# Performance work log

Hardware: AMD Instinct MI355X
Metric: run time of the kernel (lower is better)

## Reference

```python
import jax, jax.numpy as jnp
import numpy as np

N = 30000
E = 480000
D_IN = 128
EPS = 1e-5
NEG_SLOPE = 0.2
# (in_dim, out_channels, heads) per GATConv layer; concat=True everywhere (PyG default)
CFG = [(D_IN, 100, 5), (500, 50, 5), (250, 32, 4), (128, 8, 4), (32, 1, 1)]
BN_DIMS = (500, 250, 128)


def setup_inputs() -> dict:
    key = jax.random.key(0)
    ks = iter(jax.random.split(key, 80))
    inp = {
        "x": jax.random.normal(next(ks), (N, D_IN), jnp.float32),
        "edge_index": jax.random.randint(next(ks), (2, E), 0, N),
        "edge_weight": jax.random.uniform(next(ks), (E, 1), jnp.float32),
    }
    for l, (cin, cout, h) in enumerate(CFG, 1):
        s = 1.0 / np.sqrt(cin)
        inp[f"W{l}"] = jax.random.normal(next(ks), (cin, h * cout), jnp.float32) * s
        inp[f"a_s{l}"] = jax.random.normal(next(ks), (1, h, cout), jnp.float32) * 0.1
        inp[f"a_d{l}"] = jax.random.normal(next(ks), (1, h, cout), jnp.float32) * 0.1
        inp[f"We{l}"] = jax.random.normal(next(ks), (1, h * cout), jnp.float32)
        inp[f"a_e{l}"] = jax.random.normal(next(ks), (1, h, cout), jnp.float32) * 0.1
        inp[f"b{l}"] = jnp.zeros((h * cout,), jnp.float32)
    for l, d in zip((1, 2, 3), BN_DIMS):
        inp[f"g{l}"] = jnp.ones((d,), jnp.float32)
        inp[f"beta{l}"] = jnp.zeros((d,), jnp.float32)
    return inp


def _gat(x, src, dst, ea, W, a_s, a_d, We, a_e, b, heads, cout):
    """PyG GATConv with edge_dim attention (concat=True)."""
    n = x.shape[0]
    h = (x @ W).reshape(n, heads, cout)            # [N,H,C]
    e = (ea @ We).reshape(-1, heads, cout)         # [E,H,C]
    al_src = (h * a_s).sum(-1)                     # [N,H]
    al_dst = (h * a_d).sum(-1)                     # [N,H]
    logit = jax.nn.leaky_relu(al_src[src] + al_dst[dst] + (e * a_e).sum(-1), NEG_SLOPE)
    m = jax.ops.segment_max(logit, dst, num_segments=n)
    m = jnp.where(jnp.isfinite(m), m, 0.0)
    ex = jnp.exp(logit - m[dst])                   # [E,H]
    den = jax.ops.segment_sum(ex, dst, num_segments=n)
    alpha = ex / jnp.maximum(den[dst], 1e-16)      # segment softmax over in-edges of dst
    out = jax.ops.segment_sum(h[src] * alpha[..., None], dst, num_segments=n)
    return out.reshape(n, heads * cout) + b


def _bn(x, g, b):
    mu = x.mean(0)
    var = x.var(0)  # biased, as torch uses for normalization
    return (x - mu) * jax.lax.rsqrt(var + EPS) * g + b


def reference(x, edge_index, edge_weight,
              W1, a_s1, a_d1, We1, a_e1, b1,
              W2, a_s2, a_d2, We2, a_e2, b2,
              W3, a_s3, a_d3, We3, a_e3, b3,
              W4, a_s4, a_d4, We4, a_e4, b4,
              W5, a_s5, a_d5, We5, a_e5, b5,
              g1, beta1, g2, beta2, g3, beta3):
    # add self loops (PyG default) with edge_attr fill_value='mean'
    loop = jnp.arange(N)
    src = jnp.concatenate([edge_index[0], loop])
    dst = jnp.concatenate([edge_index[1], loop])
    ea = jnp.concatenate([edge_weight, jnp.full((N, 1), edge_weight.mean(), edge_weight.dtype)], axis=0)

    h = _gat(x, src, dst, ea, W1, a_s1, a_d1, We1, a_e1, b1, 5, 100)
    h = jax.nn.relu(_bn(h, g1, beta1))
    h = _gat(h, src, dst, ea, W2, a_s2, a_d2, We2, a_e2, b2, 5, 50)
    h = jax.nn.relu(_bn(h, g2, beta2))
    h = _gat(h, src, dst, ea, W3, a_s3, a_d3, We3, a_e3, b3, 4, 32)
    h = jax.nn.relu(_bn(h, g3, beta3))
    h = _gat(h, src, dst, ea, W4, a_s4, a_d4, We4, a_e4, b4, 4, 8)
    h = jax.nn.relu(h)
    h = _gat(h, src, dst, ea, W5, a_s5, a_d5, We5, a_e5, b5, 1, 1)
    return h
```

## Files before the change

### kernel.cpp

```cpp
#include <hip/hip_runtime.h>
#include <hip/hip_bf16.h>
#include <math.h>

#define NN 30000
#define EE 480000
#define ET (EE + NN)
#define NEG_SLOPE 0.2f
#define BN_EPS 1e-5f

struct LayerCfg { int cin, C, H; };
static const LayerCfg g_cfg[5] = {
    {128, 100, 5}, {500, 50, 5}, {250, 32, 4}, {128, 8, 4}, {32, 1, 1}
};

typedef short short8 __attribute__((ext_vector_type(8)));
typedef float f32x4 __attribute__((ext_vector_type(4)));

__device__ __forceinline__ unsigned short f2bf(float f) {
    unsigned int u = __builtin_bit_cast(unsigned int, f);
    u = (u + 0x7FFFu + ((u >> 16) & 1u)) >> 16;
    return (unsigned short)u;
}
__device__ __forceinline__ float bf2f(unsigned short h) {
    unsigned int u = ((unsigned int)h) << 16;
    return __builtin_bit_cast(float, u);
}


struct PrepArgs {
    const float* W[5];
    const float* We[5];
    const float* ae[5];
    unsigned short* bh[5];
    unsigned short* bl[5];
    float* wedot;
    int K[5], N[5], Kp[5], Np[5], C[5], H[5];
};

static const int EBLK = (ET + 255) / 256;

__global__ void prep_fused_kernel(const int* __restrict__ ei, int* __restrict__ rank,
                                  int* __restrict__ cnt, const float* __restrict__ ew,
                                  float* __restrict__ esum, PrepArgs a) {
    __shared__ float sdata[256];
    __shared__ float tile[32][33];
    int b = blockIdx.x;
    int tid = threadIdx.x;

    if (b < EBLK) {
        int e = b * 256 + tid;
        if (e < ET) {
            int d = (e < EE) ? ei[EE + e] : (e - EE);
            rank[e] = atomicAdd(&cnt[d], 1);
        }
        return;
    }
    b -= EBLK;
    if (b < 256) {
        float s = 0.f;
        for (int i = b * 256 + tid; i < EE; i += 65536)
            s += ew[i];
        sdata[tid] = s;
        __syncthreads();
        for (int off = 128; off > 0; off >>= 1) {
            if (tid < off) sdata[tid] += sdata[tid + off];
            __syncthreads();
        }
        if (tid == 0) atomicAdd(esum, sdata[0]);
        return;
    }
    b -= 256;
    int bx = b & 15, by = (b >> 4) & 15, bz = b >> 8;
    int l = bz;
    int tx = tid & 31, ty = tid >> 5;
    if (bx == 0 && by == 0 && ty == 0 && tx < 8) {
        int hd = tx;
        if (hd < a.H[l]) {
            int C = a.C[l];
            const float* We = a.We[l] + hd * C;
            const float* ae = a.ae[l] + hd * C;
            float s = 0.f;
            for (int c = 0; c < C; c++) s += We[c] * ae[c];
            a.wedot[l * 8 + hd] = s;
        }
    }
    int Kp = a.Kp[l], Np = a.Np[l], K = a.K[l], N = a.N[l];
    int kb = bx * 32, nb = by * 32;
    if (kb >= Kp || nb >= Np) return;
    const float* B = a.W[l];
    unsigned short* Bth = a.bh[l];
    unsigned short* Btl = a.bl[l];
#pragma unroll
    for (int i = 0; i < 4; i++) {
        int k = kb + ty + i * 8, n = nb + tx;
        tile[ty + i * 8][tx] = (k < K && n < N) ? B[(size_t)k * N + n] : 0.f;
    }
    __syncthreads();
#pragma unroll
    for (int i = 0; i < 4; i++) {
        int n = nb + ty + i * 8, k = kb + tx;
        if (n < Np && k < Kp) {
            float v = tile[tx][ty + i * 8];
            unsigned short hi = f2bf(v);
            unsigned short lo = f2bf(v - bf2f(hi));
            size_t idx = (size_t)n * Kp + k;
            Bth[idx] = hi;
            Btl[idx] = lo;
        }
    }
}

__global__ void scan_kernel(const int* __restrict__ cnt, int* __restrict__ off) {
    __shared__ int lsum[1024];
    const int T = 1024;
    int t = threadIdx.x;
    int chunk = (NN + T - 1) / T;
    int base = t * chunk;
    int end = min(NN, base + chunk);
    int s = 0;
    for (int i = base; i < end; i++) s += cnt[i];
    lsum[t] = s;
    __syncthreads();
    for (int d = 1; d < T; d <<= 1) {
        int v = (t >= d) ? lsum[t - d] : 0;
        __syncthreads();
        lsum[t] += v;
        __syncthreads();
    }
    int run = (t == 0) ? 0 : lsum[t - 1];
    for (int i = base; i < end; i++) {
        off[i] = run;
        run += cnt[i];
    }
    if (t == 0) off[NN] = ET;
}

__global__ void fill_kernel(const int* __restrict__ ei, const int* __restrict__ rank,
                            const float* __restrict__ ew, const float* __restrict__ esum,
                            const int* __restrict__ off,
                            int* __restrict__ csr_src, float* __restrict__ csr_ea) {
    int e = blockIdx.x * blockDim.x + threadIdx.x;
    if (e >= ET) return;
    int sv, d;
    if (e < EE) { sv = ei[e]; d = ei[EE + e]; }
    else        { sv = e - EE; d = e - EE; }
    int p = off[d] + rank[e];
    csr_src[p] = sv;
    csr_ea[p]  = (e < EE) ? ew[e] : esum[0] * (1.0f / (float)EE);
}

#define GBM 128
#define GBNT 128
#define GBK 32
#define ASTR 36
__global__ __launch_bounds__(256) void gemm_split_kernel(const float* __restrict__ A,
                                                         const unsigned short* __restrict__ Bt_hi,
                                                         const unsigned short* __restrict__ Bt_lo,
                                                         float* __restrict__ Cm,
                                                         unsigned short* __restrict__ Ch16,
                                                         int M, int Kp, int Nc,
                                                         const float* __restrict__ colsum,
                                                         const float* __restrict__ colsumsq,
                                                         const float* __restrict__ g,
                                                         const float* __restrict__ beta,
                                                         int D) {
    __shared__ short AsH[GBM * ASTR];
    __shared__ short AsL[GBM * ASTR];
    __shared__ short BsH[GBNT * ASTR];
    __shared__ short BsL[GBNT * ASTR];
    __shared__ float sscale[512];
    __shared__ float sshift[512];
    int tid = threadIdx.x;
    bool bn = (colsum != nullptr);
    if (bn) {
        for (int c = tid; c < Kp; c += 256) {
            float sc = 0.f, sh = 0.f;
            if (c < D) {
                float mu = colsum[c] * (1.0f / (float)NN);
                float var = colsumsq[c] * (1.0f / (float)NN) - mu * mu;
                sc = g[c] * rsqrtf(var + BN_EPS);
                sh = beta[c] - mu * sc;
            }
            sscale[c] = sc;
            sshift[c] = sh;
        }
        __syncthreads();
    }
    int wave = tid >> 6, lane = tid & 63;
    int q = lane >> 4, r = lane & 15;
    int m0 = blockIdx.y * GBM, n0 = blockIdx.x * GBNT;
    int wm = (wave & 1) * 64, wn = (wave >> 1) * 64;
    f32x4 acc[4][4];
#pragma unroll
    for (int i = 0; i < 4; i++)
#pragma unroll
        for (int j = 0; j < 4; j++) acc[i][j] = (f32x4)(0.f);

    int arow2 = tid >> 1;
    int acol2 = (tid & 1) * 16;
    int brow = tid >> 2;
    int bcol = (tid & 3) * 8;

    int ksteps = Kp / GBK;
    for (int ks = 0; ks < ksteps; ks++) {
        int k0 = ks * GBK;
        {
            int m = m0 + arow2;
            float v[16];
            if (m < M) {
                const float* Ap = A + (size_t)m * Kp + k0 + acol2;
                float4 f0 = *(const float4*)(Ap);
                float4 f1 = *(const float4*)(Ap + 4);
                float4 f2 = *(const float4*)(Ap + 8);
                float4 f3 = *(const float4*)(Ap + 12);
                v[0]=f0.x; v[1]=f0.y; v[2]=f0.z; v[3]=f0.w;
                v[4]=f1.x; v[5]=f1.y; v[6]=f1.z; v[7]=f1.w;
                v[8]=f2.x; v[9]=f2.y; v[10]=f2.z; v[11]=f2.w;
                v[12]=f3.x; v[13]=f3.y; v[14]=f3.z; v[15]=f3.w;
                if (bn) {
                    int cb = k0 + acol2;
#pragma unroll
                    for (int i = 0; i < 16; i++)
                        v[i] = fmaxf(v[i] * sscale[cb + i] + sshift[cb + i], 0.f);
                }
            } else {
#pragma unroll
                for (int i = 0; i < 16; i++) v[i] = 0.f;
            }
#pragma unroll
            for (int i = 0; i < 16; i++) {
                unsigned short hi = f2bf(v[i]);
                unsigned short lo = f2bf(v[i] - bf2f(hi));
                AsH[arow2 * ASTR + acol2 + i] = (short)hi;
                AsL[arow2 * ASTR + acol2 + i] = (short)lo;
            }
        }
#pragma unroll
        for (int p = 0; p < 2; p++) {
            int row = p * 64 + brow;
            size_t gidx = (size_t)(n0 + row) * Kp + k0 + bcol;
            *((uint4*)(BsH + row * ASTR + bcol)) = *((const uint4*)(Bt_hi + gidx));
            *((uint4*)(BsL + row * ASTR + bcol)) = *((const uint4*)(Bt_lo + gidx));
        }
        __syncthreads();
        short8 ah[4], al[4], bh[4], bl[4];
#pragma unroll
        for (int i = 0; i < 4; i++) {
            ah[i] = *((const short8*)(AsH + (wm + i * 16 + r) * ASTR + q * 8));
            al[i] = *((const short8*)(AsL + (wm + i * 16 + r) * ASTR + q * 8));
        }
#pragma unroll
        for (int j = 0; j < 4; j++) {
            bh[j] = *((const short8*)(BsH + (wn + j * 16 + r) * ASTR + q * 8));
            bl[j] = *((const short8*)(BsL + (wn + j * 16 + r) * ASTR + q * 8));
        }
#pragma unroll
        for (int i = 0; i < 4; i++)
#pragma unroll
            for (int j = 0; j < 4; j++) {
                acc[i][j] = __builtin_amdgcn_mfma_f32_16x16x32_bf16(ah[i], bh[j], acc[i][j], 0, 0, 0);
                acc[i][j] = __builtin_amdgcn_mfma_f32_16x16x32_bf16(ah[i], bl[j], acc[i][j], 0, 0, 0);
                acc[i][j] = __builtin_amdgcn_mfma_f32_16x16x32_bf16(al[i], bh[j], acc[i][j], 0, 0, 0);
            }
        __syncthreads();
    }
#pragma unroll
    for (int i = 0; i < 4; i++) {
#pragma unroll
        for (int j = 0; j < 4; j++) {
#pragma unroll
            for (int reg = 0; reg < 4; reg++) {
                int mrow = m0 + wm + i * 16 + q * 4 + reg;
                int ncol = n0 + wn + j * 16 + r;
                if (mrow < M && ncol < Nc) {
                    float val = acc[i][j][reg];
                    if (Cm)   Cm[(size_t)mrow * Nc + ncol] = val;
                    if (Ch16) Ch16[(size_t)mrow * Nc + ncol] = f2bf(val);
                }
            }
        }
    }
}

__global__ void gemv_l5_kernel(const float* __restrict__ X, const float* __restrict__ W,
                               const float* __restrict__ a_s, const float* __restrict__ a_d,
                               float* __restrict__ h, float* __restrict__ al_src,
                               float* __restrict__ al_dst) {
    __shared__ float w[32];
    if (threadIdx.x < 32) w[threadIdx.x] = W[threadIdx.x];
    __syncthreads();
    int n = blockIdx.x * blockDim.x + threadIdx.x;
    if (n >= NN) return;
    const float* row = X + (size_t)n * 32;
    float s = 0.f;
#pragma unroll
    for (int i = 0; i < 8; i++) {
        float4 f = *(const float4*)(row + i * 4);
        s += f.x * w[i * 4] + f.y * w[i * 4 + 1] + f.z * w[i * 4 + 2] + f.w * w[i * 4 + 3];
    }
    h[n] = s;
    al_src[n] = s * a_s[0];
    al_dst[n] = s * a_d[0];
}

__global__ void al_wave_h16_kernel(const unsigned short* __restrict__ h16,
                                   const float* __restrict__ a_s,
                                   const float* __restrict__ a_d,
                                   float* __restrict__ al_src, float* __restrict__ al_dst,
                                   int H, int C, int HCp) {
    int w = (blockIdx.x * blockDim.x + threadIdx.x) >> 6;
    int lane = threadIdx.x & 63;
    if (w >= NN) return;
    const unsigned short* row = h16 + (size_t)w * HCp;
    float s1[5] = {0.f, 0.f, 0.f, 0.f, 0.f};
    float s2[5] = {0.f, 0.f, 0.f, 0.f, 0.f};
#pragma unroll
    for (int hd = 0; hd < 5; hd++) {
        if (hd >= H) break;
        int base = hd * C;
        for (int c = lane * 2; c < C; c += 128) {
            unsigned int u = *(const unsigned int*)(row + base + c);
            float v0 = bf2f((unsigned short)(u & 0xffffu));
            float v1 = bf2f((unsigned short)(u >> 16));
            s1[hd] += v0 * a_s[base + c] + v1 * a_s[base + c + 1];
            s2[hd] += v0 * a_d[base + c] + v1 * a_d[base + c + 1];
        }
    }
#pragma unroll
    for (int hd = 0; hd < 5; hd++) {
        if (hd >= H) break;
#pragma unroll
        for (int off = 32; off > 0; off >>= 1) {
            s1[hd] += __shfl_xor(s1[hd], off, 64);
            s2[hd] += __shfl_xor(s2[hd], off, 64);
        }
    }
    if (lane == 0) {
#pragma unroll
        for (int hd = 0; hd < 5; hd++) {
            if (hd >= H) break;
            al_src[(size_t)w * H + hd] = s1[hd];
            al_dst[(size_t)w * H + hd] = s2[hd];
        }
    }
}

__global__ void attn_kernel(const float* __restrict__ al_src,
                            const float* __restrict__ al_dst,
                            const int* __restrict__ csr_src,
                            const float* __restrict__ csr_ea,
                            const float* __restrict__ we_dot,
                            const int* __restrict__ off,
                            float* __restrict__ alpha_t,
                            float* __restrict__ inv_den, int H, int NH) {
    int t = blockIdx.x * blockDim.x + threadIdx.x;
    if (t >= NH) return;
    int n = t / H, hd = t - n * H;
    int s = off[n], e = off[n + 1];
    float ad = al_dst[(size_t)n * H + hd];
    float wd = we_dot[hd];
    float* arow = alpha_t + (size_t)hd * ET;
    float den = 0.f;
    int p = s;
    for (; p + 3 < e; p += 4) {
        int s0 = csr_src[p], s1 = csr_src[p + 1], s2 = csr_src[p + 2], s3 = csr_src[p + 3];
        float w0 = csr_ea[p], w1 = csr_ea[p + 1], w2 = csr_ea[p + 2], w3 = csr_ea[p + 3];
        float l0 = al_src[(size_t)s0 * H + hd] + ad + w0 * wd;
        float l1 = al_src[(size_t)s1 * H + hd] + ad + w1 * wd;
        float l2 = al_src[(size_t)s2 * H + hd] + ad + w2 * wd;
        float l3 = al_src[(size_t)s3 * H + hd] + ad + w3 * wd;
        l0 = (l0 >= 0.f) ? l0 : NEG_SLOPE * l0;
        l1 = (l1 >= 0.f) ? l1 : NEG_SLOPE * l1;
        l2 = (l2 >= 0.f) ? l2 : NEG_SLOPE * l2;
        l3 = (l3 >= 0.f) ? l3 : NEG_SLOPE * l3;
        float e0 = __expf(l0), e1 = __expf(l1), e2 = __expf(l2), e3 = __expf(l3);
        arow[p] = e0; arow[p + 1] = e1; arow[p + 2] = e2; arow[p + 3] = e3;
        den += e0 + e1 + e2 + e3;
    }
    for (; p < e; p++) {
        float lg = al_src[(size_t)csr_src[p] * H + hd] + ad + csr_ea[p] * wd;
        lg = (lg >= 0.f) ? lg : NEG_SLOPE * lg;
        float ex = __expf(lg);
        arow[p] = ex;
        den += ex;
    }
    inv_den[t] = 1.f / fmaxf(den, 1e-16f);
}

#define AGG_T 64
#define IDX_STR 68
#define AL_ROW 68
__global__ void aggregate_slab_lds_kernel(const unsigned short* __restrict__ h16,
                                          const float* __restrict__ alpha_t,
                                          const int* __restrict__ off,
                                          const int* __restrict__ csr_src,
                                          const float* __restrict__ bias,
                                          const float* __restrict__ inv_den,
                                          float* __restrict__ out,
                                          int C, int H, int HC, int hp,
                                          int lns, int lcps, int npr, int nhs,
                                          int algstr, int tight, int relu, int opitch) {
    extern __shared__ char smem[];
    int cps = 1 << lcps;
    int G = 256 >> lcps;
    int* sidx = (int*)smem;
    float* sal = (float*)(smem + (size_t)G * IDX_STR * 4);
    __shared__ int s_maxt;

    int vs = blockIdx.x & 7;
    int nb = blockIdx.x >> 3;
    int slab = vs & ((1 << lns) - 1);
    int rep  = vs >> lns;
    int tid = threadIdx.x;
    int lc = tid & (cps - 1);
    int g = tid >> lcps;
    int nl = nb * G + g;
    bool active = (nl < npr);
    int n = rep * npr + (active ? nl : 0);

    int slab_j = slab << (lcps + 2);
    int j = slab_j + (lc << 2);
    int hlo = slab_j / C;
    int hhi = (slab_j + (cps << 2) - 1) / C;
    if (hhi > H - 1) hhi = H - 1;
    int nval = hhi - hlo + 1;

    int hdA = j / C;
    int hdB = (j + 3) / C;
    int bnd = (hdA + 1) * C - j;
    bnd = (bnd > 4) ? 4 : bnd;
    int selA = hdA - hlo; if (selA >= nhs) selA = nhs - 1;
    int selB = hdB - hlo; if (selB >= nhs) selB = nhs - 1;
    int hA = (hdA < H) ? hdA : H - 1;
    int hB = (hdB < H) ? hdB : H - 1;

    int s = active ? off[n] : 0;
    int e = active ? off[n + 1] : 0;
    int nt = (e - s + AGG_T - 1) / AGG_T;

    if (tid == 0) s_maxt = 0;
    __syncthreads();
    if (lc == 0 && active && nt > 0) atomicMax(&s_maxt, nt);
    __syncthreads();
    int maxt = s_maxt;

    int hpb = hp << 1;
    const char* hb = (const char*)(h16 + j);
    int* myidx = sidx + g * IDX_STR;
    float* myal = sal + (size_t)g * algstr;
    float ac0 = 0.f, ac1 = 0.f, ac2 = 0.f, ac3 = 0.f;

    for (int t = 0; t < maxt; t++) {
        int base = s + t * AGG_T;
        int cnt = e - base;
        if (cnt < 0) cnt = 0;
        if (cnt > AGG_T) cnt = AGG_T;
        __syncthreads();
        for (int q = lc; q < cnt; q += cps)
            myidx[q] = csr_src[base + q] * hpb;
        for (int r = 0; r < nhs; r++) {
            bool hv = (r < nval);
            const float* ar = alpha_t + (size_t)(hlo + r) * ET;
            float* dst = myal + r * AL_ROW;
            for (int q = lc; q < cnt; q += cps)
                dst[q] = hv ? ar[base + q] : 0.f;
        }
        __syncthreads();
        if (tight) {
            const float* aA = myal + selA * AL_ROW;
            int q = 0;
            for (; q + 3 < cnt; q += 4) {
                int b0 = myidx[q], b1 = myidx[q + 1], b2 = myidx[q + 2], b3 = myidx[q + 3];
                float a0 = aA[q], a1 = aA[q + 1], a2 = aA[q + 2], a3 = aA[q + 3];
                ushort4 u0 = *(const ushort4*)(hb + b0);
                ushort4 u1 = *(const ushort4*)(hb + b1);
                ushort4 u2 = *(const ushort4*)(hb + b2);
                ushort4 u3 = *(const ushort4*)(hb + b3);
                ac0 += a0 * bf2f(u0.x); ac1 += a0 * bf2f(u0.y);
                ac2 += a0 * bf2f(u0.z); ac3 += a0 * bf2f(u0.w);
                ac0 += a1 * bf2f(u1.x); ac1 += a1 * bf2f(u1.y);
                ac2 += a1 * bf2f(u1.z); ac3 += a1 * bf2f(u1.w);
                ac0 += a2 * bf2f(u2.x); ac1 += a2 * bf2f(u2.y);
                ac2 += a2 * bf2f(u2.z); ac3 += a2 * bf2f(u2.w);
                ac0 += a3 * bf2f(u3.x); ac1 += a3 * bf2f(u3.y);
                ac2 += a3 * bf2f(u3.z); ac3 += a3 * bf2f(u3.w);
            }
            for (; q < cnt; q++) {
                int b0 = myidx[q];
                float a0 = aA[q];
                ushort4 uv = *(const ushort4*)(hb + b0);
                ac0 += a0 * bf2f(uv.x); ac1 += a0 * bf2f(uv.y);
                ac2 += a0 * bf2f(uv.z); ac3 += a0 * bf2f(uv.w);
            }
        } else {
            const float* aA = myal + selA * AL_ROW;
            const float* aB = myal + selB * AL_ROW;
            int q = 0;
            for (; q + 3 < cnt; q += 4) {
                int b0 = myidx[q], b1 = myidx[q + 1], b2 = myidx[q + 2], b3 = myidx[q + 3];
                float a0 = aA[q], a1 = aA[q + 1], a2 = aA[q + 2], a3 = aA[q + 3];
                float c0 = aB[q], c1 = aB[q + 1], c2 = aB[q + 2], c3 = aB[q + 3];
                ushort4 u0 = *(const ushort4*)(hb + b0);
                ushort4 u1 = *(const ushort4*)(hb + b1);
                ushort4 u2 = *(const ushort4*)(hb + b2);
                ushort4 u3 = *(const ushort4*)(hb + b3);
                ac0 += ((0 < bnd) ? a0 : c0) * bf2f(u0.x);
                ac1 += ((1 < bnd) ? a0 : c0) * bf2f(u0.y);
                ac2 += ((2 < bnd) ? a0 : c0) * bf2f(u0.z);
                ac3 += ((3 < bnd) ? a0 : c0) * bf2f(u0.w);
                ac0 += ((0 < bnd) ? a1 : c1) * bf2f(u1.x);
                ac1 += ((1 < bnd) ? a1 : c1) * bf2f(u1.y);
                ac2 += ((2 < bnd) ? a1 : c1) * bf2f(u1.z);
                ac3 += ((3 < bnd) ? a1 : c1) * bf2f(u1.w);
                ac0 += ((0 < bnd) ? a2 : c2) * bf2f(u2.x);
                ac1 += ((1 < bnd) ? a2 : c2) * bf2f(u2.y);
                ac2 += ((2 < bnd) ? a2 : c2) * bf2f(u2.z);
                ac3 += ((3 < bnd) ? a2 : c2) * bf2f(u2.w);
                ac0 += ((0 < bnd) ? a3 : c3) * bf2f(u3.x);
                ac1 += ((1 < bnd) ? a3 : c3) * bf2f(u3.y);
                ac2 += ((2 < bnd) ? a3 : c3) * bf2f(u3.z);
                ac3 += ((3 < bnd) ? a3 : c3) * bf2f(u3.w);
            }
            for (; q < cnt; q++) {
                int b0 = myidx[q];
                float a0 = aA[q], c0 = aB[q];
                ushort4 uv = *(const ushort4*)(hb + b0);
                ac0 += ((0 < bnd) ? a0 : c0) * bf2f(uv.x);
                ac1 += ((1 < bnd) ? a0 : c0) * bf2f(uv.y);
                ac2 += ((2 < bnd) ? a0 : c0) * bf2f(uv.z);
                ac3 += ((3 < bnd) ? a0 : c0) * bf2f(uv.w);
            }
        }
    }
    if (!active) return;
    float invA = inv_den[(size_t)n * H + hA];
    float invB = inv_den[(size_t)n * H + hB];
    float o0 = ac0 * ((0 < bnd) ? invA : invB) + ((j + 0 < HC) ? bias[j + 0] : 0.f);
    float o1 = ac1 * ((1 < bnd) ? invA : invB) + ((j + 1 < HC) ? bias[j + 1] : 0.f);
    float o2 = ac2 * ((2 < bnd) ? invA : invB) + ((j + 2 < HC) ? bias[j + 2] : 0.f);
    float o3 = ac3 * ((3 < bnd) ? invA : invB) + ((j + 3 < HC) ? bias[j + 3] : 0.f);
    if (relu) {
        o0 = fmaxf(o0, 0.f); o1 = fmaxf(o1, 0.f);
        o2 = fmaxf(o2, 0.f); o3 = fmaxf(o3, 0.f);
    }
    *(float4*)(out + (size_t)n * opitch + j) = make_float4(o0, o1, o2, o3);
}

__global__ void aggregate_kernel(const float* __restrict__ hfeat,
                                 const float* __restrict__ alpha_t,
                                 const int* __restrict__ off, const int* __restrict__ csr_src,
                                 const float* __restrict__ bias,
                                 const float* __restrict__ inv_den,
                                 float* __restrict__ out, int total) {
    int t = blockIdx.x * blockDim.x + threadIdx.x;
    if (t >= total) return;
    int n = t;
    int s = off[n], e = off[n + 1];
    float acc = 0.f;
    int p = s;
    for (; p + 3 < e; p += 4) {
        acc += alpha_t[p] * hfeat[csr_src[p]]
             + alpha_t[p + 1] * hfeat[csr_src[p + 1]]
             + alpha_t[p + 2] * hfeat[csr_src[p + 2]]
             + alpha_t[p + 3] * hfeat[csr_src[p + 3]];
    }
    for (; p < e; p++) acc += alpha_t[p] * hfeat[csr_src[p]];
    out[n] = acc * inv_den[n] + bias[0];
}


__global__ void bn_stats_kernel(const float* __restrict__ x, float* __restrict__ colsum,
                                float* __restrict__ colsumsq, int D, int pitch) {
    int rows_per_block = (NN + gridDim.x - 1) / gridDim.x;
    int r0 = blockIdx.x * rows_per_block;
    int r1 = min(NN, r0 + rows_per_block);
    int c0 = threadIdx.x;
    int c1 = threadIdx.x + 256;
    float s0 = 0.f, q0 = 0.f, s1 = 0.f, q1 = 0.f;
    for (int r = r0; r < r1; r++) {
        const float* row = x + (size_t)r * pitch;
        if (c0 < D) { float v = row[c0]; s0 += v; q0 += v * v; }
        if (c1 < D) { float v = row[c1]; s1 += v; q1 += v * v; }
    }
    if (c0 < D) { atomicAdd(&colsum[c0], s0); atomicAdd(&colsumsq[c0], q0); }
    if (c1 < D) { atomicAdd(&colsum[c1], s1); atomicAdd(&colsumsq[c1], q1); }
}


static inline size_t align_up(size_t v, size_t a) { return (v + a - 1) / a * a; }

extern "C" void kernel_launch(void* const* d_in, const int* in_sizes, int n_in,
                              void* d_out, int out_size, void* d_ws, size_t ws_size,
                              hipStream_t stream) {
    const float* x_in = (const float*)d_in[0];
    const int* ei     = (const int*)d_in[1];
    const float* ew   = (const float*)d_in[2];

    char* pws = (char*)d_ws;
    size_t off_b = 0;
    auto alloc = [&](size_t bytes) -> void* {
        void* rp = pws + off_b;
        off_b = align_up(off_b + bytes, 256);
        return rp;
    };
    float* B0      = (float*)alloc((size_t)NN * 4);
    float* B1      = (float*)alloc((size_t)NN * 512 * 4);
    unsigned short* H16 = (unsigned short*)alloc((size_t)NN * 512 * 2);
    float* alpha_t = (float*)alloc((size_t)ET * 5 * 4);
    unsigned short* Wt_hi = (unsigned short*)alloc((size_t)600 * 512 * 2);
    unsigned short* Wt_lo = (unsigned short*)alloc((size_t)600 * 512 * 2);
    float* al_src  = (float*)alloc((size_t)NN * 5 * 4);
    float* al_dst  = (float*)alloc((size_t)NN * 5 * 4);
    float* inv_den = (float*)alloc((size_t)NN * 5 * 4);
    float* csr_ea  = (float*)alloc((size_t)ET * 4);
    int* rankb     = (int*)alloc((size_t)ET * 4);
    int* csr_src   = (int*)alloc((size_t)ET * 4);
    int* offarr    = (int*)alloc((size_t)(NN + 1) * 4);
    float* we_dot  = (float*)alloc(40 * 4);
    float* esum    = (float*)alloc(4);
    int* cnt       = (int*)alloc((size_t)NN * 4);
    float* colsum_all   = (float*)alloc(3 * 512 * 4);
    float* colsumsq_all = (float*)alloc(3 * 512 * 4);
    char* zero_end = pws + off_b;
    (void)ws_size; (void)n_in; (void)in_sizes; (void)out_size;

    int Kp[5], Np[5], hp[5];
    size_t wtoff[5];
    size_t acc_off = 0;
    for (int l = 0; l < 5; l++) {
        int K = g_cfg[l].cin, HC = g_cfg[l].C * g_cfg[l].H;
        Kp[l] = (K + 31) / 32 * 32;
        Np[l] = (HC + 127) / 128 * 128;
        hp[l] = (HC >= 64) ? ((HC + 63) / 64 * 64) : ((HC + 7) / 8 * 8);
        wtoff[l] = acc_off;
        acc_off += (size_t)Kp[l] * Np[l];
    }

    PrepArgs pa;
    for (int l = 0; l < 5; l++) {
        pa.W[l]  = (const float*)d_in[3 + l * 6 + 0];
        pa.We[l] = (const float*)d_in[3 + l * 6 + 3];
        pa.ae[l] = (const float*)d_in[3 + l * 6 + 4];
        pa.bh[l] = Wt_hi + wtoff[l];
        pa.bl[l] = Wt_lo + wtoff[l];
        pa.K[l] = g_cfg[l].cin;
        pa.N[l] = g_cfg[l].C * g_cfg[l].H;
        pa.Kp[l] = Kp[l];
        pa.Np[l] = Np[l];
        pa.C[l] = g_cfg[l].C;
        pa.H[l] = g_cfg[l].H;
    }
    pa.wedot = we_dot;

    hipMemsetAsync(esum, 0, (size_t)(zero_end - (char*)esum), stream);
    int ebl = EBLK;
    prep_fused_kernel<<<ebl + 256 + 1280, 256, 0, stream>>>(ei, rankb, cnt, ew, esum, pa);
    scan_kernel<<<1, 1024, 0, stream>>>(cnt, offarr);
    fill_kernel<<<ebl, 256, 0, stream>>>(ei, rankb, ew, esum, offarr, csr_src, csr_ea);

    for (int l = 0; l < 5; l++) {
        const LayerCfg& cf = g_cfg[l];
        int H = cf.H, C = cf.C;
        int HC = H * C;
        const float* a_s = (const float*)d_in[3 + l * 6 + 1];
        const float* a_d = (const float*)d_in[3 + l * 6 + 2];
        const float* b   = (const float*)d_in[3 + l * 6 + 5];

        const float* X = (l == 0) ? x_in : B1;
        float* outbuf = (l == 4) ? (float*)d_out : B1;
        int opitch = (l == 4) ? 1 : Kp[l + 1];
        int NH = NN * H;
        int alblocks = (NN * 64 + 255) / 256;

        if (l == 4) {
            gemv_l5_kernel<<<(NN + 255) / 256, 256, 0, stream>>>(
                X, pa.W[4], a_s, a_d, B0, al_src, al_dst);
        } else {
            const float* cs = (l >= 1) ? colsum_all + (l - 1) * 512 : nullptr;
            const float* cq = (l >= 1) ? colsumsq_all + (l - 1) * 512 : nullptr;
            const float* gg = (l >= 1) ? (const float*)d_in[33 + (l - 1) * 2 + 0] : nullptr;
            const float* bb = (l >= 1) ? (const float*)d_in[33 + (l - 1) * 2 + 1] : nullptr;
            int Din = (l >= 1) ? g_cfg[l - 1].C * g_cfg[l - 1].H : 0;
            dim3 ggrid(Np[l] / GBNT, (NN + GBM - 1) / GBM);
            gemm_split_kernel<<<ggrid, 256, 0, stream>>>(X, Wt_hi + wtoff[l], Wt_lo + wtoff[l],
                                                         nullptr, H16,
                                                         NN, Kp[l], hp[l], cs, cq, gg, bb, Din);
            al_wave_h16_kernel<<<alblocks, 256, 0, stream>>>(H16, a_s, a_d, al_src, al_dst, H, C, hp[l]);
        }

        attn_kernel<<<(NH + 255) / 256, 256, 0, stream>>>(al_src, al_dst, csr_src, csr_ea,
                                                          we_dot + l * 8, offarr, alpha_t,
                                                          inv_den, H, NH);

        if (l == 4) {
            aggregate_kernel<<<(NN + 255) / 256, 256, 0, stream>>>(
                B0, alpha_t, offarr, csr_src, b, inv_den, outbuf, NN);
        } else {
            int cps = (hp[l] >= 64) ? 16 : 8;
            int lcps = (cps == 16) ? 4 : 3;
            int slabcols = cps * 4;
            int nslabs = hp[l] / slabcols;
            int lns = (nslabs == 8) ? 3 : (nslabs == 4) ? 2 : (nslabs == 2) ? 1 : 0;
            int dup = 8 / nslabs;
            int npr = NN / dup;
            int G = 256 / cps;
            int gx = 8 * ((npr + G - 1) / G);
            int nhs = 1;
            for (int sbi = 0; sbi < nslabs; sbi++) {
                int j0 = sbi * slabcols;
                int span = (j0 + slabcols - 1) / C - j0 / C + 1;
                if (span > nhs) nhs = span;
            }
            int algstr = nhs * AL_ROW + 4;
            int tight = ((C & 3) == 0) ? 1 : 0;
            size_t smem = (size_t)G * IDX_STR * 4 + (size_t)G * algstr * 4;
            aggregate_slab_lds_kernel<<<gx, 256, smem, stream>>>(
                H16, alpha_t, offarr, csr_src, b, inv_den, outbuf,
                C, H, HC, hp[l], lns, lcps, npr, nhs, algstr, tight,
                (l == 3) ? 1 : 0, opitch);
        }

        if (l < 3) {
            bn_stats_kernel<<<512, 256, 0, stream>>>(outbuf, colsum_all + l * 512,
                                                     colsumsq_all + l * 512, HC, opitch);
        }
    }
}
```

Measured before the change: 742.3 us.

## Fuse BN column statistics into aggregation and add 8-wide slab kernel for layer 3

Removes the separate bn_stats pass by accumulating per-column sum and sum-of-squares in LDS atomics inside the aggregation kernels, then flushing them to global with atomics. This saves a full re-read of each layer output. It also adds an aggregation variant for layer 3 where each lane gathers 8 bf16 columns with 16-byte loads. The cost is extra LDS atomic contention and a block-wide sync at the end of aggregation, plus global float atomics that make the summation order nondeterministic.

```diff
diff --git a/kernel.cpp b/kernel.cpp
--- a/kernel.cpp
+++ b/kernel.cpp
@@ -24,6 +24,12 @@
 __device__ __forceinline__ float bf2f(unsigned short h) {
     unsigned int u = ((unsigned int)h) << 16;
     return __builtin_bit_cast(float, u);
+}
+__device__ __forceinline__ float bf_lo(unsigned int d) {
+    return __builtin_bit_cast(float, d << 16);
+}
+__device__ __forceinline__ float bf_hi(unsigned int d) {
+    return __builtin_bit_cast(float, d & 0xffff0000u);
 }
 
 
@@ -399,13 +405,18 @@
                                           float* __restrict__ out,
                                           int C, int H, int HC, int hp,
                                           int lns, int lcps, int npr, int nhs,
-                                          int algstr, int tight, int relu, int opitch) {
+                                          int algstr, int tight,
+                                          float* __restrict__ cs_out,
+                                          float* __restrict__ cq_out,
+                                          int relu, int opitch) {
     extern __shared__ char smem[];
     int cps = 1 << lcps;
     int G = 256 >> lcps;
     int* sidx = (int*)smem;
     float* sal = (float*)(smem + (size_t)G * IDX_STR * 4);
     __shared__ int s_maxt;
+    __shared__ float bn_s[64];
+    __shared__ float bn_q[64];
 
     int vs = blockIdx.x & 7;
     int nb = blockIdx.x >> 3;
@@ -439,6 +450,7 @@
     int nt = (e - s + AGG_T - 1) / AGG_T;
 
     if (tid == 0) s_maxt = 0;
+    if (tid < 64) { bn_s[tid] = 0.f; bn_q[tid] = 0.f; }
     __syncthreads();
     if (lc == 0 && active && nt > 0) atomicMax(&s_maxt, nt);
     __syncthreads();
@@ -532,18 +544,171 @@
             }
         }
     }
-    if (!active) return;
     float invA = inv_den[(size_t)n * H + hA];
     float invB = inv_den[(size_t)n * H + hB];
     float o0 = ac0 * ((0 < bnd) ? invA : invB) + ((j + 0 < HC) ? bias[j + 0] : 0.f);
     float o1 = ac1 * ((1 < bnd) ? invA : invB) + ((j + 1 < HC) ? bias[j + 1] : 0.f);
     float o2 = ac2 * ((2 < bnd) ? invA : invB) + ((j + 2 < HC) ? bias[j + 2] : 0.f);
     float o3 = ac3 * ((3 < bnd) ? invA : invB) + ((j + 3 < HC) ? bias[j + 3] : 0.f);
+    if (cs_out) {
+        if (active) {
+            int cb = lc << 2;
+            atomicAdd(&bn_s[cb + 0], o0); atomicAdd(&bn_q[cb + 0], o0 * o0);
+            atomicAdd(&bn_s[cb + 1], o1); atomicAdd(&bn_q[cb + 1], o1 * o1);
+            atomicAdd(&bn_s[cb + 2], o2); atomicAdd(&bn_q[cb + 2], o2 * o2);
+            atomicAdd(&bn_s[cb + 3], o3); atomicAdd(&bn_q[cb + 3], o3 * o3);
+        }
+        __syncthreads();
+        int sc = 1 << (lcps + 2);
+        if (tid < sc) {
+            atomicAdd(&cs_out[slab_j + tid], bn_s[tid]);
+            atomicAdd(&cq_out[slab_j + tid], bn_q[tid]);
+        }
+    }
+    if (!active) return;
     if (relu) {
         o0 = fmaxf(o0, 0.f); o1 = fmaxf(o1, 0.f);
         o2 = fmaxf(o2, 0.f); o3 = fmaxf(o3, 0.f);
     }
     *(float4*)(out + (size_t)n * opitch + j) = make_float4(o0, o1, o2, o3);
+}
+
+__global__ void aggregate_slab8_kernel(const unsigned short* __restrict__ h16,
+                                       const float* __restrict__ alpha_t,
+                                       const int* __restrict__ off,
+                                       const int* __restrict__ csr_src,
+                                       const float* __restrict__ bias,
+                                       const float* __restrict__ inv_den,
+                                       float* __restrict__ out,
+                                       int C, int H, int HC, int hp,
+                                       int lns, int npr, int nhs, int algstr,
+                                       float* __restrict__ cs_out,
+                                       float* __restrict__ cq_out,
+                                       int relu, int opitch) {
+    extern __shared__ char smem[];
+    const int cps = 8, G = 32;
+    int* sidx = (int*)smem;
+    float* sal = (float*)(smem + (size_t)G * IDX_STR * 4);
+    __shared__ int s_maxt;
+    __shared__ float bn_s[64];
+    __shared__ float bn_q[64];
+
+    int vs = blockIdx.x & 7;
+    int nb = blockIdx.x >> 3;
+    int slab = vs & ((1 << lns) - 1);
+    int rep  = vs >> lns;
+    int tid = threadIdx.x;
+    int lc = tid & 7;
+    int g = tid >> 3;
+    int nl = nb * G + g;
+    bool active = (nl < npr);
+    int n = rep * npr + (active ? nl : 0);
+
+    int slab_j = slab << 6;
+    int j = slab_j + (lc << 3);
+    int hlo = slab_j / C;
+    int hd = j / C;
+    int sel = hd - hlo; if (sel >= nhs) sel = nhs - 1;
+    int hcl = (hd < H) ? hd : H - 1;
+
+    int s = active ? off[n] : 0;
+    int e = active ? off[n + 1] : 0;
+    int nt = (e - s + AGG_T - 1) / AGG_T;
+    int hhi = (slab_j + 63) / C;
+    if (hhi > H - 1) hhi = H - 1;
+    int nval = hhi - hlo + 1;
+
+    if (tid == 0) s_maxt = 0;
+    if (tid < 64) { bn_s[tid] = 0.f; bn_q[tid] = 0.f; }
+    __syncthreads();
+    if (lc == 0 && active && nt > 0) atomicMax(&s_maxt, nt);
+    __syncthreads();
+    int maxt = s_maxt;
+
+    int hpb = hp << 1;
+    const char* hb = (const char*)(h16 + j);
+    int* myidx = sidx + g * IDX_STR;
+    float* myal = sal + (size_t)g * algstr;
+    float ac0 = 0.f, ac1 = 0.f, ac2 = 0.f, ac3 = 0.f;
+    float ac4 = 0.f, ac5 = 0.f, ac6 = 0.f, ac7 = 0.f;
+
+    for (int t = 0; t < maxt; t++) {
+        int base = s + t * AGG_T;
+        int cnt = e - base;
+        if (cnt < 0) cnt = 0;
+        if (cnt > AGG_T) cnt = AGG_T;
+        __syncthreads();
+        for (int q = lc; q < cnt; q += cps)
+            myidx[q] = csr_src[base + q] * hpb;
+        for (int r = 0; r < nhs; r++) {
+            bool hv = (r < nval);
+            const float* ar = alpha_t + (size_t)(hlo + r) * ET;
+            float* dst = myal + r * AL_ROW;
+            for (int q = lc; q < cnt; q += cps)
+                dst[q] = hv ? ar[base + q] : 0.f;
+        }
+        __syncthreads();
+        const float* aA = myal + sel * AL_ROW;
+        int q = 0;
+        for (; q + 1 < cnt; q += 2) {
+            int b0 = myidx[q], b1 = myidx[q + 1];
+            float a0 = aA[q], a1 = aA[q + 1];
+            uint4 u0 = *(const uint4*)(hb + b0);
+            uint4 u1 = *(const uint4*)(hb + b1);
+            ac0 += a0 * bf_lo(u0.x); ac1 += a0 * bf_hi(u0.x);
+            ac2 += a0 * bf_lo(u0.y); ac3 += a0 * bf_hi(u0.y);
+            ac4 += a0 * bf_lo(u0.z); ac5 += a0 * bf_hi(u0.z);
+            ac6 += a0 * bf_lo(u0.w); ac7 += a0 * bf_hi(u0.w);
+            ac0 += a1 * bf_lo(u1.x); ac1 += a1 * bf_hi(u1.x);
+            ac2 += a1 * bf_lo(u1.y); ac3 += a1 * bf_hi(u1.y);
+            ac4 += a1 * bf_lo(u1.z); ac5 += a1 * bf_hi(u1.z);
+            ac6 += a1 * bf_lo(u1.w); ac7 += a1 * bf_hi(u1.w);
+        }
+        for (; q < cnt; q++) {
+            int b0 = myidx[q];
+            float a0 = aA[q];
+            uint4 uv = *(const uint4*)(hb + b0);
+            ac0 += a0 * bf_lo(uv.x); ac1 += a0 * bf_hi(uv.x);
+            ac2 += a0 * bf_lo(uv.y); ac3 += a0 * bf_hi(uv.y);
+            ac4 += a0 * bf_lo(uv.z); ac5 += a0 * bf_hi(uv.z);
+            ac6 += a0 * bf_lo(uv.w); ac7 += a0 * bf_hi(uv.w);
+        }
+    }
+    float inv = inv_den[(size_t)n * H + hcl];
+    float o0 = ac0 * inv + ((j + 0 < HC) ? bias[j + 0] : 0.f);
+    float o1 = ac1 * inv + ((j + 1 < HC) ? bias[j + 1] : 0.f);
+    float o2 = ac2 * inv + ((j + 2 < HC) ? bias[j + 2] : 0.f);
+    float o3 = ac3 * inv + ((j + 3 < HC) ? bias[j + 3] : 0.f);
+    float o4 = ac4 * inv + ((j + 4 < HC) ? bias[j + 4] : 0.f);
+    float o5 = ac5 * inv + ((j + 5 < HC) ? bias[j + 5] : 0.f);
+    float o6 = ac6 * inv + ((j + 6 < HC) ? bias[j + 6] : 0.f);
+    float o7 = ac7 * inv + ((j + 7 < HC) ? bias[j + 7] : 0.f);
+    if (cs_out) {
+        if (active) {
+            int cb = lc << 3;
+            atomicAdd(&bn_s[cb + 0], o0); atomicAdd(&bn_q[cb + 0], o0 * o0);
+            atomicAdd(&bn_s[cb + 1], o1); atomicAdd(&bn_q[cb + 1], o1 * o1);
+            atomicAdd(&bn_s[cb + 2], o2); atomicAdd(&bn_q[cb + 2], o2 * o2);
+            atomicAdd(&bn_s[cb + 3], o3); atomicAdd(&bn_q[cb + 3], o3 * o3);
+            atomicAdd(&bn_s[cb + 4], o4); atomicAdd(&bn_q[cb + 4], o4 * o4);
+            atomicAdd(&bn_s[cb + 5], o5); atomicAdd(&bn_q[cb + 5], o5 * o5);
+            atomicAdd(&bn_s[cb + 6], o6); atomicAdd(&bn_q[cb + 6], o6 * o6);
+            atomicAdd(&bn_s[cb + 7], o7); atomicAdd(&bn_q[cb + 7], o7 * o7);
+        }
+        __syncthreads();
+        if (tid < 64) {
+            atomicAdd(&cs_out[slab_j + tid], bn_s[tid]);
+            atomicAdd(&cq_out[slab_j + tid], bn_q[tid]);
+        }
+    }
+    if (!active) return;
+    if (relu) {
+        o0 = fmaxf(o0, 0.f); o1 = fmaxf(o1, 0.f); o2 = fmaxf(o2, 0.f); o3 = fmaxf(o3, 0.f);
+        o4 = fmaxf(o4, 0.f); o5 = fmaxf(o5, 0.f); o6 = fmaxf(o6, 0.f); o7 = fmaxf(o7, 0.f);
+    }
+    float* op = out + (size_t)n * opitch + j;
+    *(float4*)(op)     = make_float4(o0, o1, o2, o3);
+    *(float4*)(op + 4) = make_float4(o4, o5, o6, o7);
 }
 
 __global__ void aggregate_kernel(const float* __restrict__ hfeat,
@@ -566,24 +731,6 @@
     }
     for (; p < e; p++) acc += alpha_t[p] * hfeat[csr_src[p]];
     out[n] = acc * inv_den[n] + bias[0];
-}
-
-
-__global__ void bn_stats_kernel(const float* __restrict__ x, float* __restrict__ colsum,
-                                float* __restrict__ colsumsq, int D, int pitch) {
-    int rows_per_block = (NN + gridDim.x - 1) / gridDim.x;
-    int r0 = blockIdx.x * rows_per_block;
-    int r1 = min(NN, r0 + rows_per_block);
-    int c0 = threadIdx.x;
-    int c1 = threadIdx.x + 256;
-    float s0 = 0.f, q0 = 0.f, s1 = 0.f, q1 = 0.f;
-    for (int r = r0; r < r1; r++) {
-        const float* row = x + (size_t)r * pitch;
-        if (c0 < D) { float v = row[c0]; s0 += v; q0 += v * v; }
-        if (c1 < D) { float v = row[c1]; s1 += v; q1 += v * v; }
-    }
-    if (c0 < D) { atomicAdd(&colsum[c0], s0); atomicAdd(&colsumsq[c0], q0); }
-    if (c1 < D) { atomicAdd(&colsum[c1], s1); atomicAdd(&colsumsq[c1], q1); }
 }
 
 
@@ -692,9 +839,30 @@
                                                           we_dot + l * 8, offarr, alpha_t,
                                                           inv_den, H, NH);
 
+        float* csO = (l < 3) ? colsum_all + l * 512 : nullptr;
+        float* cqO = (l < 3) ? colsumsq_all + l * 512 : nullptr;
+
         if (l == 4) {
             aggregate_kernel<<<(NN + 255) / 256, 256, 0, stream>>>(
                 B0, alpha_t, offarr, csr_src, b, inv_den, outbuf, NN);
+        } else if (l == 2) {
+            int nslabs = hp[l] / 64;
+            int lns = (nslabs == 2) ? 1 : 0;
+            int dup = 8 / nslabs;
+            int npr = NN / dup;
+            int G = 32;
+            int gx = 8 * ((npr + G - 1) / G);
+            int nhs = 1;
+            for (int sbi = 0; sbi < nslabs; sbi++) {
+                int j0 = sbi * 64;
+                int span = (j0 + 63) / C - j0 / C + 1;
+                if (span > nhs) nhs = span;
+            }
+            int algstr = nhs * AL_ROW + 4;
+            size_t smem = (size_t)G * IDX_STR * 4 + (size_t)G * algstr * 4;
+            aggregate_slab8_kernel<<<gx, 256, smem, stream>>>(
+                H16, alpha_t, offarr, csr_src, b, inv_den, outbuf,
+                C, H, HC, hp[l], lns, npr, nhs, algstr, csO, cqO, 0, opitch);
         } else {
             int cps = (hp[l] >= 64) ? 16 : 8;
             int lcps = (cps == 16) ? 4 : 3;
@@ -717,12 +885,7 @@
             aggregate_slab_lds_kernel<<<gx, 256, smem, stream>>>(
                 H16, alpha_t, offarr, csr_src, b, inv_den, outbuf,
                 C, H, HC, hp[l], lns, lcps, npr, nhs, algstr, tight,
-                (l == 3) ? 1 : 0, opitch);
-        }
-
-        if (l < 3) {
-            bn_stats_kernel<<<512, 256, 0, stream>>>(outbuf, colsum_all + l * 512,
-                                                     colsumsq_all + l * 512, HC, opitch);
-        }
-    }
-}
+                csO, cqO, (l == 3) ? 1 : 0, opitch);
+        }
+    }
+}
```

After: 871.7 us. +17.4%, slower.
